# Kernel tuning notes

Measured on AMD Instinct MI355X. Metric: run time of the kernel, lower is better.

The kernel has to match this reference:

```python
import jax, jax.numpy as jnp
import numpy as np

K = 16  # knn


def conv1x1(x, w, b):
    # x: (B,Cin,k,N), w: (Cout,Cin), b: (Cout,)
    return jnp.einsum('oc,bckn->bokn', w, x) + b[None, :, None, None]


def leaky(x):
    return jnp.where(x >= 0, x, 0.2 * x)


def conv_res(x, sc_w, sc_b, a_w, a_b, b_w, b_b, c_w, c_b):
    sc = conv1x1(x, sc_w, sc_b)
    h = leaky(conv1x1(x, a_w, a_b))
    h = leaky(conv1x1(h, b_w, b_b))
    h = conv1x1(h, c_w, c_b)
    return h + sc


def get_knn_feature(xyz, k):
    # xyz: (B,3,N) -> feature (B,10,k,N)
    x_t = jnp.transpose(xyz, (0, 2, 1))  # (B,N,3)
    xx = jnp.sum(x_t * x_t, axis=-1)  # (B,N)
    inner = jnp.einsum('bnc,bmc->bnm', x_t, x_t)  # (B,N,N)
    d2 = xx[:, :, None] + xx[:, None, :] - 2.0 * inner  # squared dists
    _, idx = jax.lax.top_k(-d2, k)  # (B,N,k) nearest (includes self)
    neighbors = jax.vmap(lambda pts, i: pts[i])(x_t, idx)  # (B,N,k,3)
    center = x_t[:, :, None, :]  # (B,N,1,3)
    rel = neighbors - center
    dist = jnp.sqrt(jnp.sum(rel * rel, axis=-1, keepdims=True) + 1e-12)  # (B,N,k,1)
    feat = jnp.concatenate([jnp.broadcast_to(center, neighbors.shape), neighbors, rel, dist], axis=-1)  # (B,N,k,10)
    return jnp.transpose(feat, (0, 3, 2, 1))  # (B,10,k,N)


def _mk_w(key, o, i):
    s = 1.0 / np.sqrt(i)
    return jax.random.uniform(key, (o, i), jnp.float32, -s, s)


def setup_inputs():
    key = jax.random.key(0)
    ks = jax.random.split(key, 20)
    B, N = 4, 8192
    hide, out = 64, 128
    inp = {'xyz': jax.random.normal(ks[0], (B, 3, N), jnp.float32)}
    # CONV_Res(10, 64, 64)
    inp['p1_sc_w'] = _mk_w(ks[1], hide, 10); inp['p1_sc_b'] = jnp.zeros((hide,), jnp.float32)
    inp['p1_a_w'] = _mk_w(ks[2], hide, 10); inp['p1_a_b'] = jnp.zeros((hide,), jnp.float32)
    inp['p1_b_w'] = _mk_w(ks[3], hide, hide); inp['p1_b_b'] = jnp.zeros((hide,), jnp.float32)
    inp['p1_c_w'] = _mk_w(ks[4], hide, hide); inp['p1_c_b'] = jnp.zeros((hide,), jnp.float32)
    # CONV_Res(128, 64, 128)
    inp['p2_sc_w'] = _mk_w(ks[5], out, 2 * hide); inp['p2_sc_b'] = jnp.zeros((out,), jnp.float32)
    inp['p2_a_w'] = _mk_w(ks[6], hide, 2 * hide); inp['p2_a_b'] = jnp.zeros((hide,), jnp.float32)
    inp['p2_b_w'] = _mk_w(ks[7], out, hide); inp['p2_b_b'] = jnp.zeros((out,), jnp.float32)
    inp['p2_c_w'] = _mk_w(ks[8], out, out); inp['p2_c_b'] = jnp.zeros((out,), jnp.float32)
    return inp


def reference(xyz, p1_sc_w, p1_sc_b, p1_a_w, p1_a_b, p1_b_w, p1_b_b, p1_c_w, p1_c_b,
              p2_sc_w, p2_sc_b, p2_a_w, p2_a_b, p2_b_w, p2_b_b, p2_c_w, p2_c_b):
    x = get_knn_feature(xyz, K)  # (B,10,k,N)
    x = conv_res(x, p1_sc_w, p1_sc_b, p1_a_w, p1_a_b, p1_b_w, p1_b_b, p1_c_w, p1_c_b)  # (B,64,k,N)
    x1 = jnp.max(x, axis=2, keepdims=True)  # (B,64,1,N)
    x1 = jnp.broadcast_to(x1, x.shape)  # repeat over k
    x = jnp.concatenate([x, x1], axis=1)  # (B,128,k,N)
    x = conv_res(x, p2_sc_w, p2_sc_b, p2_a_w, p2_a_b, p2_b_w, p2_b_b, p2_c_w, p2_c_b)  # (B,128,k,N)
    return jnp.max(x, axis=2)  # (B,128,N)
```

## Files before the change

### kernel.cpp

```cpp
#include <hip/hip_runtime.h>
#include <hip/hip_bf16.h>

#define B_ 4
#define N_ 8192
#define KNN 16
#define BN_ (B_*N_)
#define NPOS (BN_*KNN)

typedef __attribute__((ext_vector_type(8))) short bf16x8;
typedef __attribute__((ext_vector_type(4))) float f32x4;

static __device__ __forceinline__ unsigned short f2bf(float f) {
  union { float f; unsigned u; } v; v.f = f;
  unsigned r = v.u + 0x7fff + ((v.u >> 16) & 1);
  return (unsigned short)(r >> 16);
}
static __device__ __forceinline__ float lk(float x) { return x >= 0.f ? x : 0.2f*x; }
static __device__ __forceinline__ unsigned pk2(float a, float b) {
  return (unsigned)f2bf(a) | ((unsigned)f2bf(b) << 16);
}

__global__ void k_prep(const float* __restrict__ xyz, float4* __restrict__ pts4) {
  int i = blockIdx.x * 256 + threadIdx.x;
  if (i >= BN_) return;
  int b = i >> 13, n = i & (N_-1);
  const float* p = xyz + b*3*N_;
  float x = p[n], y = p[N_+n], z = p[2*N_+n];
  float xx = fmaf(z, z, fmaf(y, y, x*x));
  pts4[i] = make_float4(x, y, z, xx);
}

__global__ void k_wcvt(const float* __restrict__ w_sc, const float* __restrict__ w_a,
                       const float* __restrict__ w_b, const float* __restrict__ w_c,
                       const float* __restrict__ p1a, const float* __restrict__ p1sc,
                       const float* __restrict__ p1b, const float* __restrict__ p1c,
                       unsigned short* __restrict__ out) {
  int i = blockIdx.x*256 + threadIdx.x;
  if (i >= 61440) return;
  if (i < 49152) {
    int x = i*2;
    const float* w; int base, K2;
    if (x < 32768)      { w = w_sc; base = 0;     K2 = 256; }
    else if (x < 49152) { w = w_a;  base = 32768; K2 = 256; }
    else if (x < 65536) { w = w_b;  base = 49152; K2 = 128; }
    else                { w = w_c;  base = 65536; K2 = 256; }
    int off = x - base;
    int row = off / K2;
    int colb = (off & (K2-1)) ^ ((row & 7) << 4);
    int k = colb >> 1;
    out[i] = f2bf(w[row*(K2 >> 1) + k]);
  } else {
    int e = i - 49152;
    float val; int byteoff;
    if (e < 2048) {
      int row = e >> 5, k = e & 31;
      val = (k < 10) ? p1a[row*10 + k] : 0.f;
      byteoff = row*64 + ((2*k) ^ ((row & 3) << 4));
    } else if (e < 4096) {
      int le = e - 2048, row = le >> 5, k = le & 31;
      val = (k < 10) ? p1sc[row*10 + k] : 0.f;
      byteoff = 4096 + row*64 + ((2*k) ^ ((row & 3) << 4));
    } else if (e < 8192) {
      int le = e - 4096, row = le >> 6, k = le & 63;
      val = p1b[row*64 + k];
      byteoff = 8192 + row*128 + ((2*k) ^ ((row & 7) << 4));
    } else {
      int le = e - 8192, row = le >> 6, k = le & 63;
      val = p1c[row*64 + k];
      byteoff = 16384 + row*128 + ((2*k) ^ ((row & 7) << 4));
    }
    out[49152 + (byteoff >> 1)] = f2bf(val);
  }
}

__global__ __launch_bounds__(512) void k_knn(const float4* __restrict__ pts4,
                                             int* __restrict__ knn) {
  __shared__ float4 cand[2048];
  const int lane = threadIdx.x & 63;
  const int wv   = threadIdx.x >> 6;
  const int q = blockIdx.x * 8 + wv;
  const int b = q >> 13;
  const int n = q & (N_-1);
  const float4* __restrict__ P = pts4 + (b << 13);
  float4 me = P[n];

  float av = __builtin_inff(); int ai = 0;
  float worst = __builtin_inff();

  for (int ch = 0; ch < 4; ++ch) {
    __syncthreads();
    #pragma unroll
    for (int t = 0; t < 4; ++t)
      cand[t*512 + threadIdx.x] = P[ch*2048 + t*512 + threadIdx.x];
    __syncthreads();

    int it0 = 0;
    if (ch == 0) {
      float4 c = cand[lane];
      float dot = fmaf(me.z, c.z, fmaf(me.y, c.y, me.x*c.x));
      float v = (me.w + c.w) - 2.0f*dot;
      int id = lane;
      #pragma unroll
      for (int size = 2; size <= 64; size <<= 1) {
        #pragma unroll
        for (int stride = size >> 1; stride >= 1; stride >>= 1) {
          float ov = __shfl_xor(v, stride);
          int   oi = __shfl_xor(id, stride);
          bool up = ((lane & size) == 0);
          bool keepmin = (((lane & stride) == 0) == up);
          bool oless = (ov < v) || (ov == v && oi < id);
          if (oless == keepmin) { v = ov; id = oi; }
        }
      }
      av = (lane < 16) ? v : __builtin_inff();
      ai = id;
      worst = __shfl(av, 15);
      it0 = 1;
    }

    for (int it = it0; it < 32; ++it) {
      int ci = it*64 + lane;
      float4 c = cand[ci];
      float dot = fmaf(me.z, c.z, fmaf(me.y, c.y, me.x*c.x));
      float d2 = (me.w + c.w) - 2.0f*dot;
      int cid = ch*2048 + ci;
      unsigned long long m = __ballot(d2 < worst);
      if (m) {
        do {
          int src = __ffsll(m) - 1;
          m &= (m - 1);
          float v = __shfl(d2, src);
          int  id = __shfl(cid, src);
          int p = __popcll(__ballot((lane < 16) && (av <= v)));
          if (p < 16) {
            float pav = __shfl_up(av, 1);
            int   pai = __shfl_up(ai, 1);
            if (lane >= p) { av = (lane == p) ? v : pav; ai = (lane == p) ? id : pai; }
          }
        } while (m);
        worst = __shfl(av, 15);
      }
    }
  }
  if (lane < 16) knn[(q << 4) + lane] = ai;
}

__global__ __launch_bounds__(512, 4) void k_p1(
    const float4* __restrict__ pts4, const int* __restrict__ knn,
    const unsigned short* __restrict__ wbf,
    const float* __restrict__ a_b, const float* __restrict__ b_b,
    const float* __restrict__ c_b, const float* __restrict__ sc_b,
    unsigned short* __restrict__ X, unsigned short* __restrict__ XM) {
  __shared__ __align__(16) unsigned short Ws1[12288];
  __shared__ __align__(16) unsigned short Fs[8192];
  __shared__ __align__(16) unsigned short Hr[16384];
  const int tid = threadIdx.x;
  const int lane = tid & 63, wv = tid >> 6;
  const int colr = lane & 15, kq = lane >> 4;

  #pragma unroll
  for (int j = 0; j < 3; ++j) {
    int c = j*512 + tid;
    ((uint4*)Ws1)[c] = ((const uint4*)(wbf + 49152))[c];
  }
  const char* WS = (const char*)Ws1;
  char* H = (char*)Hr + wv*4096;

  for (int tile = 0; tile < 4; ++tile) {
    const int bn0 = (blockIdx.x*4 + tile) * 16;
    __syncthreads();
    if (tid < 256) {
      int bnl = tid >> 4, kk = tid & 15;
      int bn = bn0 + bnl;
      int b = bn >> 13;
      float4 cp = pts4[bn];
      int nid = knn[bn*16 + kk];
      float4 np = pts4[(b << 13) + nid];
      float rx = np.x - cp.x, ry = np.y - cp.y, rz = np.z - cp.z;
      float dist = sqrtf(fmaf(rz, rz, fmaf(ry, ry, rx*rx)) + 1e-12f);
      unsigned short row[32];
      row[0]=f2bf(cp.x); row[1]=f2bf(cp.y); row[2]=f2bf(cp.z);
      row[3]=f2bf(np.x); row[4]=f2bf(np.y); row[5]=f2bf(np.z);
      row[6]=f2bf(rx);   row[7]=f2bf(ry);   row[8]=f2bf(rz);   row[9]=f2bf(dist);
      #pragma unroll
      for (int j = 10; j < 32; ++j) row[j] = 0;
      int wvp = tid >> 5, posl = tid & 31;
      char* dst = (char*)Fs + wvp*2048 + posl*64;
      #pragma unroll
      for (int c = 0; c < 4; ++c)
        *(uint4*)(dst + ((c*16) ^ ((posl&3)<<4))) = *(const uint4*)(row + c*8);
    }
    __syncthreads();

    bf16x8 bfr[2];
    #pragma unroll
    for (int ct = 0; ct < 2; ++ct) {
      int posl = ct*16 + colr;
      bfr[ct] = *(const bf16x8*)((const char*)Fs + wv*2048 + posl*64 + ((kq*16) ^ ((posl&3)<<4)));
    }

    f32x4 acc[4][2];
    #pragma unroll
    for (int mt = 0; mt < 4; ++mt) {
      int r0 = mt*16 + kq*4;
      #pragma unroll
      for (int r = 0; r < 4; ++r) {
        float bia = c_b[r0+r] + sc_b[r0+r];
        acc[mt][0][r] = bia; acc[mt][1][r] = bia;
      }
    }
    #pragma unroll
    for (int mt = 0; mt < 4; ++mt) {
      int row = mt*16 + colr;
      bf16x8 w = *(const bf16x8*)(WS + 4096 + row*64 + ((kq*16) ^ ((row&3)<<4)));
      acc[mt][0] = __builtin_amdgcn_mfma_f32_16x16x32_bf16(w, bfr[0], acc[mt][0], 0, 0, 0);
      acc[mt][1] = __builtin_amdgcn_mfma_f32_16x16x32_bf16(w, bfr[1], acc[mt][1], 0, 0, 0);
    }

    f32x4 ha[4][2];
    #pragma unroll
    for (int mt = 0; mt < 4; ++mt) {
      int r0 = mt*16 + kq*4;
      #pragma unroll
      for (int r = 0; r < 4; ++r) { ha[mt][0][r] = a_b[r0+r]; ha[mt][1][r] = a_b[r0+r]; }
    }
    #pragma unroll
    for (int mt = 0; mt < 4; ++mt) {
      int row = mt*16 + colr;
      bf16x8 w = *(const bf16x8*)(WS + row*64 + ((kq*16) ^ ((row&3)<<4)));
      ha[mt][0] = __builtin_amdgcn_mfma_f32_16x16x32_bf16(w, bfr[0], ha[mt][0], 0, 0, 0);
      ha[mt][1] = __builtin_amdgcn_mfma_f32_16x16x32_bf16(w, bfr[1], ha[mt][1], 0, 0, 0);
    }

    #pragma unroll
    for (int mt = 0; mt < 4; ++mt) {
      int ch2 = (mt*16 + kq*4) * 2;
      #pragma unroll
      for (int ct = 0; ct < 2; ++ct) {
        int posl = ct*16 + colr;
        uint2 u;
        u.x = pk2(lk(ha[mt][ct][0]), lk(ha[mt][ct][1]));
        u.y = pk2(lk(ha[mt][ct][2]), lk(ha[mt][ct][3]));
        *(uint2*)(H + posl*128 + (ch2 ^ ((posl&7)<<4))) = u;
      }
    }
    bf16x8 bh[2][2];
    #pragma unroll
    for (int ct = 0; ct < 2; ++ct) {
      int posl = ct*16 + colr;
      #pragma unroll
      for (int k2 = 0; k2 < 2; ++k2)
        bh[ct][k2] = *(const bf16x8*)(H + posl*128 + ((k2*64 + kq*16) ^ ((posl&7)<<4)));
    }

    #pragma unroll
    for (int jj = 0; jj < 2; ++jj) {
      f32x4 h2[2][2];
      #pragma unroll
      for (int mtp = 0; mtp < 2; ++mtp) {
        int r0 = (jj*2 + mtp)*16 + kq*4;
        #pragma unroll
        for (int r = 0; r < 4; ++r) { h2[mtp][0][r] = b_b[r0+r]; h2[mtp][1][r] = b_b[r0+r]; }
      }
      #pragma unroll
      for (int mtp = 0; mtp < 2; ++mtp) {
        int row = (jj*2 + mtp)*16 + colr;
        #pragma unroll
        for (int k2 = 0; k2 < 2; ++k2) {
          bf16x8 w = *(const bf16x8*)(WS + 8192 + row*128 + ((k2*64 + kq*16) ^ ((row&7)<<4)));
          h2[mtp][0] = __builtin_amdgcn_mfma_f32_16x16x32_bf16(w, bh[0][k2], h2[mtp][0], 0, 0, 0);
          h2[mtp][1] = __builtin_amdgcn_mfma_f32_16x16x32_bf16(w, bh[1][k2], h2[mtp][1], 0, 0, 0);
        }
      }
      #pragma unroll
      for (int mtp = 0; mtp < 2; ++mtp) {
        int ch2 = ((jj*2 + mtp)*16 + kq*4) * 2;
        #pragma unroll
        for (int ct = 0; ct < 2; ++ct) {
          int posl = ct*16 + colr;
          uint2 u;
          u.x = pk2(lk(h2[mtp][ct][0]), lk(h2[mtp][ct][1]));
          u.y = pk2(lk(h2[mtp][ct][2]), lk(h2[mtp][ct][3]));
          *(uint2*)(H + posl*128 + (ch2 ^ ((posl&7)<<4))) = u;
        }
      }
      bf16x8 b2[2];
      #pragma unroll
      for (int ct = 0; ct < 2; ++ct) {
        int posl = ct*16 + colr;
        b2[ct] = *(const bf16x8*)(H + posl*128 + ((jj*64 + kq*16) ^ ((posl&7)<<4)));
      }
      #pragma unroll
      for (int mt = 0; mt < 4; ++mt) {
        int row = mt*16 + colr;
        bf16x8 w = *(const bf16x8*)(WS + 16384 + row*128 + ((jj*64 + kq*16) ^ ((row&7)<<4)));
        acc[mt][0] = __builtin_amdgcn_mfma_f32_16x16x32_bf16(w, b2[0], acc[mt][0], 0, 0, 0);
        acc[mt][1] = __builtin_amdgcn_mfma_f32_16x16x32_bf16(w, b2[1], acc[mt][1], 0, 0, 0);
      }
    }

    #pragma unroll
    for (int ct = 0; ct < 2; ++ct) {
      int bn = bn0 + wv*2 + ct;
      #pragma unroll
      for (int mt = 0; mt < 4; ++mt) {
        int ch0 = mt*16 + kq*4;
        uint2 u;
        u.x = pk2(acc[mt][ct][0], acc[mt][ct][1]);
        u.y = pk2(acc[mt][ct][2], acc[mt][ct][3]);
        *(uint2*)(X + ((size_t)(bn*16 + colr))*64 + ch0) = u;
        float m[4];
        #pragma unroll
        for (int r = 0; r < 4; ++r) {
          float v = acc[mt][ct][r];
          v = fmaxf(v, __shfl_xor(v, 1));
          v = fmaxf(v, __shfl_xor(v, 2));
          v = fmaxf(v, __shfl_xor(v, 4));
          v = fmaxf(v, __shfl_xor(v, 8));
          m[r] = v;
        }
        if (colr == 0) {
          uint2 um; um.x = pk2(m[0], m[1]); um.y = pk2(m[2], m[3]);
          *(uint2*)(XM + (size_t)bn*64 + ch0) = um;
        }
      }
    }
  }
}

struct P2Shared {
  unsigned short Ws[49152];
  unsigned short Hr[8][2048];
  float outT[128][16];
};

static __device__ __forceinline__ void p2_loadbx(
    bf16x8 (&dst)[2][4], const unsigned short* __restrict__ X,
    const unsigned short* __restrict__ XM, int bn0, int wv, int colr, int kq) {
  #pragma unroll
  for (int ct = 0; ct < 2; ++ct) {
    int bn = bn0 + wv*2 + ct;
    const unsigned short* xr = X + ((size_t)bn*16 + colr)*64 + kq*8;
    dst[ct][0] = *(const bf16x8*)(xr);
    dst[ct][1] = *(const bf16x8*)(xr + 32);
    const unsigned short* mr = XM + (size_t)bn*64 + kq*8;
    dst[ct][2] = *(const bf16x8*)(mr);
    dst[ct][3] = *(const bf16x8*)(mr + 32);
  }
}

__global__ __launch_bounds__(512, 2) void k_p2(
    const unsigned short* __restrict__ X, const unsigned short* __restrict__ XM,
    const unsigned short* __restrict__ wbf,
    const float* __restrict__ sc_b, const float* __restrict__ a_b,
    const float* __restrict__ b_b, const float* __restrict__ c_b,
    float* __restrict__ out) {
  __shared__ __align__(16) P2Shared S;
  const int tid = threadIdx.x;
  const int lane = tid & 63, wv = tid >> 6;
  const int colr = lane & 15, kq = lane >> 4;

  #pragma unroll
  for (int it = 0; it < 12; ++it) {
    int c = it*512 + tid;
    *(uint4*)((char*)S.Ws + c*16) = *(const uint4*)((const char*)wbf + c*16);
  }

  const char* WSC = (const char*)S.Ws;
  const char* WA  = (const char*)(S.Ws + 16384);
  const char* WB  = (const char*)(S.Ws + 24576);
  const char* WC  = (const char*)(S.Ws + 32768);
  char* H = (char*)S.Hr[wv];

#define WF(base, row, K2, ksbyte) \
  (*(const bf16x8*)((base) + (row)*(K2) + ((((ksbyte) + kq*16)) ^ (((row)&7)<<4))))

  bf16x8 bx[2][4], bxn[2][4];
  p2_loadbx(bx, X, XM, blockIdx.x*8*16, wv, colr, kq);
  __syncthreads();

  for (int t = 0; t < 8; ++t) {
    const int bn0 = (blockIdx.x*8 + t) * 16;

    f32x4 acc[8][2];
    #pragma unroll
    for (int mt = 0; mt < 8; ++mt) {
      int r0 = mt*16 + kq*4;
      #pragma unroll
      for (int r = 0; r < 4; ++r) {
        float bia = c_b[r0+r] + sc_b[r0+r];
        acc[mt][0][r] = bia; acc[mt][1][r] = bia;
      }
    }
    #pragma unroll
    for (int mt = 0; mt < 8; ++mt) {
      int row = mt*16 + colr;
      #pragma unroll
      for (int ks = 0; ks < 4; ++ks) {
        bf16x8 w = WF(WSC, row, 256, ks*64);
        acc[mt][0] = __builtin_amdgcn_mfma_f32_16x16x32_bf16(w, bx[0][ks], acc[mt][0], 0, 0, 0);
        acc[mt][1] = __builtin_amdgcn_mfma_f32_16x16x32_bf16(w, bx[1][ks], acc[mt][1], 0, 0, 0);
      }
    }

    f32x4 ha[4][2];
    #pragma unroll
    for (int mt = 0; mt < 4; ++mt) {
      int r0 = mt*16 + kq*4;
      #pragma unroll
      for (int r = 0; r < 4; ++r) { ha[mt][0][r] = a_b[r0+r]; ha[mt][1][r] = a_b[r0+r]; }
    }
    #pragma unroll
    for (int mt = 0; mt < 4; ++mt) {
      int row = mt*16 + colr;
      #pragma unroll
      for (int ks = 0; ks < 4; ++ks) {
        bf16x8 w = WF(WA, row, 256, ks*64);
        ha[mt][0] = __builtin_amdgcn_mfma_f32_16x16x32_bf16(w, bx[0][ks], ha[mt][0], 0, 0, 0);
        ha[mt][1] = __builtin_amdgcn_mfma_f32_16x16x32_bf16(w, bx[1][ks], ha[mt][1], 0, 0, 0);
      }
    }

    {
      int tn = (t < 7) ? (t + 1) : 7;
      p2_loadbx(bxn, X, XM, (blockIdx.x*8 + tn) * 16, wv, colr, kq);
    }

    #pragma unroll
    for (int mt = 0; mt < 4; ++mt) {
      int ch2 = (mt*16 + kq*4) * 2;
      #pragma unroll
      for (int ct = 0; ct < 2; ++ct) {
        int posl = ct*16 + colr;
        uint2 u;
        u.x = pk2(lk(ha[mt][ct][0]), lk(ha[mt][ct][1]));
        u.y = pk2(lk(ha[mt][ct][2]), lk(ha[mt][ct][3]));
        *(uint2*)(H + posl*128 + (ch2 ^ ((posl&7)<<4))) = u;
      }
    }
    bf16x8 bh[2][2];
    #pragma unroll
    for (int ct = 0; ct < 2; ++ct) {
      int posl = ct*16 + colr;
      #pragma unroll
      for (int k2 = 0; k2 < 2; ++k2)
        bh[ct][k2] = *(const bf16x8*)(H + posl*128 + ((k2*64 + kq*16) ^ ((posl&7)<<4)));
    }

    #pragma unroll
    for (int j = 0; j < 4; ++j) {
      f32x4 h2[2][2];
      #pragma unroll
      for (int mtp = 0; mtp < 2; ++mtp) {
        int r0 = (2*j + mtp)*16 + kq*4;
        #pragma unroll
        for (int r = 0; r < 4; ++r) { h2[mtp][0][r] = b_b[r0+r]; h2[mtp][1][r] = b_b[r0+r]; }
      }
      #pragma unroll
      for (int mtp = 0; mtp < 2; ++mtp) {
        int row = (2*j + mtp)*16 + colr;
        #pragma unroll
        for (int k2 = 0; k2 < 2; ++k2) {
          bf16x8 w = WF(WB, row, 128, k2*64);
          h2[mtp][0] = __builtin_amdgcn_mfma_f32_16x16x32_bf16(w, bh[0][k2], h2[mtp][0], 0, 0, 0);
          h2[mtp][1] = __builtin_amdgcn_mfma_f32_16x16x32_bf16(w, bh[1][k2], h2[mtp][1], 0, 0, 0);
        }
      }
      char* PB = H + (j & 1)*2048;
      #pragma unroll
      for (int mtp = 0; mtp < 2; ++mtp) {
        int chp2 = (mtp*16 + kq*4) * 2;
        #pragma unroll
        for (int ct = 0; ct < 2; ++ct) {
          int posl = ct*16 + colr;
          uint2 u;
          u.x = pk2(lk(h2[mtp][ct][0]), lk(h2[mtp][ct][1]));
          u.y = pk2(lk(h2[mtp][ct][2]), lk(h2[mtp][ct][3]));
          *(uint2*)(PB + posl*64 + (chp2 ^ ((posl&3)<<4))) = u;
        }
      }
      bf16x8 b2[2];
      #pragma unroll
      for (int ct = 0; ct < 2; ++ct) {
        int posl = ct*16 + colr;
        b2[ct] = *(const bf16x8*)(PB + posl*64 + ((kq*16) ^ ((posl&3)<<4)));
      }
      #pragma unroll
      for (int mt = 0; mt < 8; ++mt) {
        int row = mt*16 + colr;
        bf16x8 w = WF(WC, row, 256, j*64);
        acc[mt][0] = __builtin_amdgcn_mfma_f32_16x16x32_bf16(w, b2[0], acc[mt][0], 0, 0, 0);
        acc[mt][1] = __builtin_amdgcn_mfma_f32_16x16x32_bf16(w, b2[1], acc[mt][1], 0, 0, 0);
      }
    }

    __syncthreads();
    #pragma unroll
    for (int mt = 0; mt < 8; ++mt) {
      #pragma unroll
      for (int ct = 0; ct < 2; ++ct) {
        #pragma unroll
        for (int r = 0; r < 4; ++r) {
          float v = acc[mt][ct][r];
          v = fmaxf(v, __shfl_xor(v, 1));
          v = fmaxf(v, __shfl_xor(v, 2));
          v = fmaxf(v, __shfl_xor(v, 4));
          v = fmaxf(v, __shfl_xor(v, 8));
          if (colr == 0) S.outT[mt*16 + kq*4 + r][wv*2 + ct] = v;
        }
      }
    }
    __syncthreads();
    {
      int ch = tid >> 2, p = tid & 3;
      int b = bn0 >> 13, n0 = bn0 & (N_-1);
      float4 v4 = *(const float4*)&S.outT[ch][p*4];
      *(float4*)(out + ((size_t)b*128 + ch)*N_ + n0 + p*4) = v4;
    }

    #pragma unroll
    for (int ct = 0; ct < 2; ++ct)
      #pragma unroll
      for (int ks = 0; ks < 4; ++ks)
        bx[ct][ks] = bxn[ct][ks];
  }
#undef WF
}

extern "C" void kernel_launch(void* const* d_in, const int* in_sizes, int n_in,
                              void* d_out, int out_size, void* d_ws, size_t ws_size,
                              hipStream_t stream) {
  const float* xyz     = (const float*)d_in[0];
  const float* p1_sc_w = (const float*)d_in[1];
  const float* p1_sc_b = (const float*)d_in[2];
  const float* p1_a_w  = (const float*)d_in[3];
  const float* p1_a_b  = (const float*)d_in[4];
  const float* p1_b_w  = (const float*)d_in[5];
  const float* p1_b_b  = (const float*)d_in[6];
  const float* p1_c_w  = (const float*)d_in[7];
  const float* p1_c_b  = (const float*)d_in[8];
  const float* p2_sc_w = (const float*)d_in[9];
  const float* p2_sc_b = (const float*)d_in[10];
  const float* p2_a_w  = (const float*)d_in[11];
  const float* p2_a_b  = (const float*)d_in[12];
  const float* p2_b_w  = (const float*)d_in[13];
  const float* p2_b_b  = (const float*)d_in[14];
  const float* p2_c_w  = (const float*)d_in[15];
  const float* p2_c_b  = (const float*)d_in[16];

  if (ws_size < 75497472u) return;
  char* ws = (char*)d_ws;
  float4* pts4        = (float4*)(ws);
  unsigned short* wbf = (unsigned short*)(ws + 524288);
  int* knn            = (int*)(ws + 655360);
  unsigned short* X   = (unsigned short*)(ws + 4194304);
  unsigned short* XM  = (unsigned short*)(ws + 4194304 + 67108864);
  float* out = (float*)d_out;

  k_prep<<<dim3(BN_/256), dim3(256), 0, stream>>>(xyz, pts4);
  k_wcvt<<<dim3(240), dim3(256), 0, stream>>>(p2_sc_w, p2_a_w, p2_b_w, p2_c_w,
      p1_a_w, p1_sc_w, p1_b_w, p1_c_w, wbf);
  k_knn<<<dim3(BN_/8), dim3(512), 0, stream>>>(pts4, knn);
  k_p1<<<dim3(512), dim3(512), 0, stream>>>(pts4, knn, wbf,
      p1_a_b, p1_b_b, p1_c_b, p1_sc_b, X, XM);
  k_p2<<<dim3(256), dim3(512), 0, stream>>>(X, XM, wbf,
      p2_sc_b, p2_a_b, p2_b_b, p2_c_b, out);
}
```

Baseline: 404.0 us.

## Batch kNN candidate insertion through shared buffer and packed-key bitonic merge

Replaces the per-candidate serial insertion into the sorted top-16 list with a per-wave shared-memory buffer. Passing candidates are compacted into the buffer with mbcnt prefix sums and merged 48 at a time by a 64-lane bitonic sort on packed (distance bits, index) 64-bit keys. The distance test is also simplified to compare against a precomputed threshold that drops the per-candidate add of the query norm. The goal is to cut the serialized shuffle-heavy insert loop. In exchange it adds shared memory and sorting work. Ordering raw float bits as unsigned would misorder any slightly negative squared distances.

```diff
diff --git a/kernel.cpp b/kernel.cpp
--- a/kernel.cpp
+++ b/kernel.cpp
@@ -73,9 +73,26 @@
   }
 }
 
+static __device__ __forceinline__ unsigned long long bitonic64(
+    unsigned long long key, int lane) {
+  #pragma unroll
+  for (int size = 2; size <= 64; size <<= 1) {
+    #pragma unroll
+    for (int stride = size >> 1; stride >= 1; stride >>= 1) {
+      unsigned long long ok = __shfl_xor((long long)key, stride);
+      bool up = ((lane & size) == 0);
+      bool keepmin = (((lane & stride) == 0) == up);
+      bool oless = ok < key;
+      if (oless == keepmin) key = ok;
+    }
+  }
+  return key;
+}
+
 __global__ __launch_bounds__(512) void k_knn(const float4* __restrict__ pts4,
                                              int* __restrict__ knn) {
   __shared__ float4 cand[2048];
+  __shared__ unsigned long long buf[8][112];
   const int lane = threadIdx.x & 63;
   const int wv   = threadIdx.x >> 6;
   const int q = blockIdx.x * 8 + wv;
@@ -84,8 +101,11 @@
   const float4* __restrict__ P = pts4 + (b << 13);
   float4 me = P[n];
 
-  float av = __builtin_inff(); int ai = 0;
+  unsigned long long topk = ~0ull;
   float worst = __builtin_inff();
+  float rhs = __builtin_inff();
+  int cnt = 0;
+  unsigned long long* __restrict__ bw = buf[wv];
 
   for (int ch = 0; ch < 4; ++ch) {
     __syncthreads();
@@ -98,23 +118,13 @@
     if (ch == 0) {
       float4 c = cand[lane];
       float dot = fmaf(me.z, c.z, fmaf(me.y, c.y, me.x*c.x));
-      float v = (me.w + c.w) - 2.0f*dot;
-      int id = lane;
-      #pragma unroll
-      for (int size = 2; size <= 64; size <<= 1) {
-        #pragma unroll
-        for (int stride = size >> 1; stride >= 1; stride >>= 1) {
-          float ov = __shfl_xor(v, stride);
-          int   oi = __shfl_xor(id, stride);
-          bool up = ((lane & size) == 0);
-          bool keepmin = (((lane & stride) == 0) == up);
-          bool oless = (ov < v) || (ov == v && oi < id);
-          if (oless == keepmin) { v = ov; id = oi; }
-        }
-      }
-      av = (lane < 16) ? v : __builtin_inff();
-      ai = id;
-      worst = __shfl(av, 15);
+      float d2 = (me.w + c.w) - 2.0f*dot;
+      unsigned long long key =
+        ((unsigned long long)__float_as_uint(d2) << 32) | (unsigned)lane;
+      topk = bitonic64(key, lane);
+      unsigned long long k15 = __shfl((long long)topk, 15);
+      worst = __uint_as_float((unsigned)(k15 >> 32));
+      rhs = worst - me.w;
       it0 = 1;
     }
 
@@ -122,27 +132,45 @@
       int ci = it*64 + lane;
       float4 c = cand[ci];
       float dot = fmaf(me.z, c.z, fmaf(me.y, c.y, me.x*c.x));
-      float d2 = (me.w + c.w) - 2.0f*dot;
-      int cid = ch*2048 + ci;
-      unsigned long long m = __ballot(d2 < worst);
+      float s = fmaf(-2.0f, dot, c.w);
+      unsigned long long m = __ballot(s < rhs);
       if (m) {
-        do {
-          int src = __ffsll(m) - 1;
-          m &= (m - 1);
-          float v = __shfl(d2, src);
-          int  id = __shfl(cid, src);
-          int p = __popcll(__ballot((lane < 16) && (av <= v)));
-          if (p < 16) {
-            float pav = __shfl_up(av, 1);
-            int   pai = __shfl_up(ai, 1);
-            if (lane >= p) { av = (lane == p) ? v : pav; ai = (lane == p) ? id : pai; }
+        int prefix = __builtin_amdgcn_mbcnt_hi((unsigned)(m >> 32),
+                      __builtin_amdgcn_mbcnt_lo((unsigned)m, 0));
+        if (s < rhs) {
+          float d2 = me.w + s;
+          bw[cnt + prefix] =
+            ((unsigned long long)__float_as_uint(d2) << 32)
+            | (unsigned)(ch*2048 + ci);
+        }
+        cnt += __popcll(m);
+        if (cnt >= 48) {
+          int base = 0;
+          while (cnt > 0) {
+            int c2 = cnt > 48 ? 48 : cnt;
+            unsigned long long e = (lane < 16) ? topk
+              : ((lane - 16) < c2 ? bw[base + lane - 16] : ~0ull);
+            topk = bitonic64(e, lane);
+            base += c2; cnt -= c2;
           }
-        } while (m);
-        worst = __shfl(av, 15);
-      }
-    }
-  }
-  if (lane < 16) knn[(q << 4) + lane] = ai;
+          unsigned long long k15 = __shfl((long long)topk, 15);
+          worst = __uint_as_float((unsigned)(k15 >> 32));
+          rhs = worst - me.w;
+        }
+      }
+    }
+  }
+  {
+    int base = 0;
+    while (cnt > 0) {
+      int c2 = cnt > 48 ? 48 : cnt;
+      unsigned long long e = (lane < 16) ? topk
+        : ((lane - 16) < c2 ? bw[base + lane - 16] : ~0ull);
+      topk = bitonic64(e, lane);
+      base += c2; cnt -= c2;
+    }
+  }
+  if (lane < 16) knn[(q << 4) + lane] = (int)(unsigned)(topk & 0xffffffffu);
 }
 
 __global__ __launch_bounds__(512, 4) void k_p1(
```

After: 403.1 us. Within noise of the previous version (-0.2%).

## Replace brute-force KNN with uniform-grid spatial hashing search

Applied to the files above, without the earlier changes.

Swaps the O(N^2) brute-force wavefront KNN for a uniform 32^3 grid. Points are binned by histogram, prefix scan and scatter into cell-sorted order, then each thread searches expanding shells of cells while keeping a per-thread sorted top-16 of packed distance/index keys, stopping once the shell bound exceeds the current worst distance. This removes most distance evaluations, but it adds several small kernels and atomics and gives divergent per-thread work that depends on the point distribution. The grid range is hardcoded to [-4,4], which fits Gaussian inputs, and the scratch buffers alias the X region, which is written only later.

```diff
diff --git a/kernel.cpp b/kernel.cpp
--- a/kernel.cpp
+++ b/kernel.cpp
@@ -73,76 +73,129 @@
   }
 }
 
-__global__ __launch_bounds__(512) void k_knn(const float4* __restrict__ pts4,
-                                             int* __restrict__ knn) {
-  __shared__ float4 cand[2048];
-  const int lane = threadIdx.x & 63;
-  const int wv   = threadIdx.x >> 6;
-  const int q = blockIdx.x * 8 + wv;
-  const int b = q >> 13;
-  const int n = q & (N_-1);
-  const float4* __restrict__ P = pts4 + (b << 13);
-  float4 me = P[n];
-
-  float av = __builtin_inff(); int ai = 0;
+#define GRES 32
+#define GC (GRES*GRES*GRES)
+#define GH 0.25f
+
+__global__ void k_zero(int* __restrict__ p, int n) {
+  int i = blockIdx.x*256 + threadIdx.x;
+  if (i < n) p[i] = 0;
+}
+
+__global__ void k_cell(const float4* __restrict__ pts4, int* __restrict__ hist,
+                       int* __restrict__ cid) {
+  int i = blockIdx.x*256 + threadIdx.x;
+  if (i >= BN_) return;
+  float4 p = pts4[i];
+  int cx = min(max((int)floorf((p.x + 4.f)*4.f), 0), GRES-1);
+  int cy = min(max((int)floorf((p.y + 4.f)*4.f), 0), GRES-1);
+  int cz = min(max((int)floorf((p.z + 4.f)*4.f), 0), GRES-1);
+  int c = (cz*GRES + cy)*GRES + cx;
+  cid[i] = c;
+  atomicAdd(&hist[(i >> 13)*GC + c], 1);
+}
+
+__global__ __launch_bounds__(1024) void k_scan(const int* __restrict__ hist,
+                                               int* __restrict__ cellStart) {
+  __shared__ int ps[1024];
+  int b = blockIdx.x, t = threadIdx.x;
+  const int* h = hist + b*GC;
+  int* cs = cellStart + b*(GC+1);
+  int loc[32]; int sum = 0;
+  #pragma unroll
+  for (int i = 0; i < 32; ++i) { loc[i] = sum; sum += h[t*32 + i]; }
+  ps[t] = sum;
+  __syncthreads();
+  for (int off = 1; off < 1024; off <<= 1) {
+    int v = (t >= off) ? ps[t - off] : 0;
+    __syncthreads();
+    ps[t] += v;
+    __syncthreads();
+  }
+  int excl = ps[t] - sum;
+  #pragma unroll
+  for (int i = 0; i < 32; ++i) cs[t*32 + i] = excl + loc[i];
+  if (t == 1023) cs[GC] = excl + sum;
+}
+
+__global__ void k_scatter(const float4* __restrict__ pts4, const int* __restrict__ cid,
+                          const int* __restrict__ cellStart, int* __restrict__ ctr,
+                          float4* __restrict__ pts_sorted, int* __restrict__ idx_sorted) {
+  int i = blockIdx.x*256 + threadIdx.x;
+  if (i >= BN_) return;
+  int b = i >> 13, c = cid[i];
+  int pos = cellStart[b*(GC+1) + c] + atomicAdd(&ctr[b*GC + c], 1);
+  int g = (b << 13) + pos;
+  pts_sorted[g] = pts4[i];
+  idx_sorted[g] = i & (N_-1);
+}
+
+__global__ __launch_bounds__(256) void k_knng(
+    const float4* __restrict__ pts4,
+    const float4* __restrict__ pts_sorted, const int* __restrict__ idx_sorted,
+    const int* __restrict__ cellStart, int* __restrict__ knn) {
+  int q = blockIdx.x*256 + threadIdx.x;
+  int b = q >> 13;
+  float4 me = pts4[q];
+  const float4* __restrict__ PS = pts_sorted + (b << 13);
+  const int* __restrict__ IS = idx_sorted + (b << 13);
+  const int* __restrict__ CS = cellStart + b*(GC+1);
+  int cx = min(max((int)floorf((me.x + 4.f)*4.f), 0), GRES-1);
+  int cy = min(max((int)floorf((me.y + 4.f)*4.f), 0), GRES-1);
+  int cz = min(max((int)floorf((me.z + 4.f)*4.f), 0), GRES-1);
+
+  unsigned long long r[16];
+  #pragma unroll
+  for (int i = 0; i < 16; ++i) r[i] = 0x7F800000FFFFFFFFull;
   float worst = __builtin_inff();
 
-  for (int ch = 0; ch < 4; ++ch) {
-    __syncthreads();
-    #pragma unroll
-    for (int t = 0; t < 4; ++t)
-      cand[t*512 + threadIdx.x] = P[ch*2048 + t*512 + threadIdx.x];
-    __syncthreads();
-
-    int it0 = 0;
-    if (ch == 0) {
-      float4 c = cand[lane];
-      float dot = fmaf(me.z, c.z, fmaf(me.y, c.y, me.x*c.x));
-      float v = (me.w + c.w) - 2.0f*dot;
-      int id = lane;
-      #pragma unroll
-      for (int size = 2; size <= 64; size <<= 1) {
-        #pragma unroll
-        for (int stride = size >> 1; stride >= 1; stride >>= 1) {
-          float ov = __shfl_xor(v, stride);
-          int   oi = __shfl_xor(id, stride);
-          bool up = ((lane & size) == 0);
-          bool keepmin = (((lane & stride) == 0) == up);
-          bool oless = (ov < v) || (ov == v && oi < id);
-          if (oless == keepmin) { v = ov; id = oi; }
-        }
-      }
-      av = (lane < 16) ? v : __builtin_inff();
-      ai = id;
-      worst = __shfl(av, 15);
-      it0 = 1;
-    }
-
-    for (int it = it0; it < 32; ++it) {
-      int ci = it*64 + lane;
-      float4 c = cand[ci];
-      float dot = fmaf(me.z, c.z, fmaf(me.y, c.y, me.x*c.x));
-      float d2 = (me.w + c.w) - 2.0f*dot;
-      int cid = ch*2048 + ci;
-      unsigned long long m = __ballot(d2 < worst);
-      if (m) {
-        do {
-          int src = __ffsll(m) - 1;
-          m &= (m - 1);
-          float v = __shfl(d2, src);
-          int  id = __shfl(cid, src);
-          int p = __popcll(__ballot((lane < 16) && (av <= v)));
-          if (p < 16) {
-            float pav = __shfl_up(av, 1);
-            int   pai = __shfl_up(ai, 1);
-            if (lane >= p) { av = (lane == p) ? v : pav; ai = (lane == p) ? id : pai; }
-          }
-        } while (m);
-        worst = __shfl(av, 15);
-      }
-    }
-  }
-  if (lane < 16) knn[(q << 4) + lane] = ai;
+#define SCAN_RANGE(st_, en_)                                                  \
+  for (int j = (st_); j < (en_); ++j) {                                      \
+    float4 c = PS[j];                                                        \
+    float dot = fmaf(me.z, c.z, fmaf(me.y, c.y, me.x*c.x));                  \
+    float d2 = me.w + fmaf(-2.f, dot, c.w);                                  \
+    if (d2 <= worst) {                                                       \
+      unsigned long long key =                                               \
+        ((unsigned long long)__float_as_uint(d2) << 32) | (unsigned)IS[j];   \
+      _Pragma("unroll")                                                      \
+      for (int i = 0; i < 16; ++i) {                                         \
+        bool sw = key < r[i];                                                \
+        unsigned long long t = r[i];                                         \
+        r[i] = sw ? key : r[i];                                              \
+        key = sw ? t : key;                                                  \
+      }                                                                      \
+      worst = __uint_as_float((unsigned)(r[15] >> 32));                      \
+    }                                                                        \
+  }
+
+  for (int s = 0; s < GRES; ++s) {
+    if (s >= 1) {
+      float bnd = (float)(s - 1) * GH;
+      if (bnd*bnd > worst) break;
+    }
+    int zlo = max(cz - s, 0), zhi = min(cz + s, GRES-1);
+    for (int z = zlo; z <= zhi; ++z) {
+      int adz = (z > cz) ? (z - cz) : (cz - z);
+      int ylo = max(cy - s, 0), yhi = min(cy + s, GRES-1);
+      for (int y = ylo; y <= yhi; ++y) {
+        int ady = (y > cy) ? (y - cy) : (cy - y);
+        int rb = (z*GRES + y)*GRES;
+        if (adz == s || ady == s) {
+          int xlo = max(cx - s, 0), xhi = min(cx + s, GRES-1);
+          int st = CS[rb + xlo], en = CS[rb + xhi + 1];
+          SCAN_RANGE(st, en)
+        } else {
+          int x0 = cx - s, x1 = cx + s;
+          if (x0 >= 0) { int st = CS[rb + x0], en = CS[rb + x0 + 1]; SCAN_RANGE(st, en) }
+          if (x1 <= GRES-1) { int st = CS[rb + x1], en = CS[rb + x1 + 1]; SCAN_RANGE(st, en) }
+        }
+      }
+    }
+  }
+#undef SCAN_RANGE
+  #pragma unroll
+  for (int i = 0; i < 16; ++i)
+    knn[q*16 + i] = (int)(unsigned)(r[i] & 0xffffffffu);
 }
 
 __global__ __launch_bounds__(512, 4) void k_p1(
@@ -555,12 +608,25 @@
   int* knn            = (int*)(ws + 655360);
   unsigned short* X   = (unsigned short*)(ws + 4194304);
   unsigned short* XM  = (unsigned short*)(ws + 4194304 + 67108864);
+  char* G = ws + 4194304;
+  int* hist        = (int*)(G);
+  int* ctr         = (int*)(G + 524288);
+  int* cid         = (int*)(G + 1048576);
+  int* cellStart   = (int*)(G + 1179648);
+  float4* psorted  = (float4*)(G + 1703952);
+  int* isorted     = (int*)(G + 2228240);
   float* out = (float*)d_out;
 
   k_prep<<<dim3(BN_/256), dim3(256), 0, stream>>>(xyz, pts4);
   k_wcvt<<<dim3(240), dim3(256), 0, stream>>>(p2_sc_w, p2_a_w, p2_b_w, p2_c_w,
       p1_a_w, p1_sc_w, p1_b_w, p1_c_w, wbf);
-  k_knn<<<dim3(BN_/8), dim3(512), 0, stream>>>(pts4, knn);
+  k_zero<<<dim3(1024), dim3(256), 0, stream>>>(hist, 2*B_*GC);
+  k_cell<<<dim3(BN_/256), dim3(256), 0, stream>>>(pts4, hist, cid);
+  k_scan<<<dim3(B_), dim3(1024), 0, stream>>>(hist, cellStart);
+  k_scatter<<<dim3(BN_/256), dim3(256), 0, stream>>>(pts4, cid, cellStart, ctr,
+      psorted, isorted);
+  k_knng<<<dim3(BN_/256), dim3(256), 0, stream>>>(pts4, psorted, isorted,
+      cellStart, knn);
   k_p1<<<dim3(512), dim3(512), 0, stream>>>(pts4, knn, wbf,
       p1_a_b, p1_b_b, p1_c_b, p1_sc_b, X, XM);
   k_p2<<<dim3(256), dim3(512), 0, stream>>>(X, XM, wbf,
```

New measurement: 815.2 us. +101.8%, slower.
